# Kernel tuning notes

Hardware: AMD Instinct MI355X
Metric: run time of the kernel (lower is better)

The kernel has to match this reference:

```python
import jax, jax.numpy as jnp
import numpy as np

RHO = 1.0
L = 50
RS = np.array([20, 40, 80, 160], dtype=np.int32)

def _get_index():
    S = []
    for m in range(-L // 2, L // 2 + 1):
        for n in range(-L // 2, L // 2 + 1):
            if abs(m * n) <= RHO * L // 2:
                S.append((m, n))
    return np.array(S, dtype=np.int32)

IDX = _get_index()          # [449, 2] (m, n) pairs
K = IDX.shape[0]            # 449
B, N, M = 8, 65536, 2       # batch, sequence length, Nmodes (dual-pol)


def setup_inputs() -> dict:
    key = jax.random.key(0)
    ks = jax.random.split(key, 8)
    shp = (B, N, M)
    inp = {
        "E_real": jax.random.normal(ks[0], shp, jnp.float32),
        "E_imag": jax.random.normal(ks[1], shp, jnp.float32),
        "F_real": jax.random.normal(ks[2], shp, jnp.float32),
        "F_imag": jax.random.normal(ks[3], shp, jnp.float32),
        "C1_real": jax.random.normal(ks[4], (len(RS), K), jnp.float32) * 0.01,
        "C1_imag": jax.random.normal(ks[5], (len(RS), K), jnp.float32) * 0.01,
        "C2_real": jax.random.normal(ks[6], (len(RS), K), jnp.float32) * 0.01,
        "C2_imag": jax.random.normal(ks[7], (len(RS), K), jnp.float32) * 0.01,
    }
    # task_info columns: (P [dBm], Fi, Fs [Hz], Nch); Fs must be 2e9 * some Rs entry
    ti = np.zeros((B, 4), dtype=np.float32)
    ti[:, 0] = 2.0
    ti[:, 2] = RS[np.arange(B) % len(RS)].astype(np.float32) * 2e9
    inp["task_info"] = jnp.asarray(ti)
    return inp


def _forward(E_real, E_imag, F_real, F_imag, C1_real, C1_imag, C2_real, C2_imag, task_info):
    E = E_real + 1j * E_imag    # [B, N, M] complex64
    F = F_real + 1j * F_imag

    # choose_C: map Fs -> row of C tables (sorted-Rs order, as in the torch code)
    rs_sorted = jnp.sort(jnp.asarray(RS))
    x = (task_info[:, 2] / 2e9).astype(jnp.int32)              # [B]
    ind = jnp.argmax(x[:, None] == rs_sorted[None, :], axis=-1)  # [B]
    C1 = (C1_real + 1j * C1_imag)[ind]                         # [B, K]
    C2 = (C2_real + 1j * C2_imag)[ind]                         # [B, K]

    ms = jnp.asarray(IDX[:, 0])
    ns = jnp.asarray(IDX[:, 1])

    def step(acc, xs):
        m, n, c1, c2 = xs                                       # c1, c2: [B]
        En  = jnp.roll(E, n, axis=-2)
        Em  = jnp.roll(E, m, axis=-2)
        Emn = jnp.roll(E, m + n, axis=-2)
        Fn  = jnp.roll(F, n, axis=-2)
        Fmn = jnp.roll(F, m + n, axis=-2)
        A = En * jnp.conj(Fmn) * c1[:, None, None] + Fn * jnp.conj(Emn) * c2[:, None, None]
        # (A + A.roll(1, dim=-1)) swaps/combines the two polarizations
        return acc + (A + jnp.roll(A, 1, axis=-1)) * Em, None

    acc, _ = jax.lax.scan(step, jnp.zeros_like(E), (ms, ns, C1.T, C2.T))

    P = jnp.power(10.0, task_info[:, 0] / 10.0) / E.shape[-1]   # [B]
    Eo = F + (jnp.sqrt(P) ** 3)[:, None, None] * acc
    return E[:, L:-L, :], Eo[:, L:-L, :]


def reference(E_real, E_imag, F_real, F_imag, C1_real, C1_imag, C2_real, C2_imag, task_info):
    return _forward(E_real, E_imag, F_real, F_imag,
                    C1_real, C1_imag, C2_real, C2_imag, task_info)
```

## Files before the change

### kernel.cpp

```cpp
#include <hip/hip_runtime.h>
#include <hip/hip_bf16.h>


namespace {

constexpr int NSEQ    = 65536;
constexpr int BATCH   = 8;
constexpr int KTAPS   = 449;
constexpr int NM      = 25;
constexpr int THREADS = 256;
constexpr int TILE    = 1024;
constexpr int WIN     = TILE + 4 * NM;
constexpr int WINQ    = WIN / 4;
constexpr int GHW     = TILE + 2 * NM + 1;
constexpr int GHH     = (GHW + 1) / 2;

typedef float v2f __attribute__((ext_vector_type(2)));

__device__ inline v2f pkfma(float s, v2f v, v2f acc) {
  return __builtin_elementwise_fma((v2f){s, s}, v, acc);
}

__device__ inline void mac(v2f& U13, v2f& U42, v2f& V13, v2f& V42,
                           const float4 c, const float4 g) {
  const v2f glo = (v2f){g.x, g.y}, ghi = (v2f){g.z, g.w};
  U13 = pkfma(c.x, glo, U13); U42 = pkfma(c.y, glo, U42);
  V13 = pkfma(c.z, ghi, V13); V42 = pkfma(c.w, ghi, V42);
}

__device__ inline unsigned short f2bf(float f) {
  __hip_bfloat16 h = __float2bfloat16(f);
  union { __hip_bfloat16 hh; unsigned short u; } cv;
  cv.hh = h;
  return cv.u;
}

__global__ void prep_c_kernel(const float* __restrict__ c1r, const float* __restrict__ c1i,
                              const float* __restrict__ c2r, const float* __restrict__ c2i,
                              float4* __restrict__ cw) {
  int idx = blockIdx.x * blockDim.x + threadIdx.x;
  if (idx < 4 * KTAPS) {
    cw[idx]             = make_float4(c1r[idx], c1i[idx], c2r[idx], c2i[idx]);
    cw[4 * KTAPS + idx] = make_float4(c2r[idx], c2i[idx], c1r[idx], c1i[idx]);
  }
}

__device__ inline float4 gh_entry(const float4 e, const float4 f,
                                  const float4 fm, const float4 em) {
  v2f G = (v2f){fm.w * e.w, fm.w * (-e.z)};
  G = pkfma(fm.x, (v2f){e.x, e.y}, G);
  G = pkfma(fm.y, (v2f){e.y, -e.x}, G);
  G = pkfma(fm.z, (v2f){e.z, e.w}, G);
  v2f H = (v2f){em.w * f.w, em.w * (-f.z)};
  H = pkfma(em.x, (v2f){f.x, f.y}, H);
  H = pkfma(em.y, (v2f){f.y, -f.x}, H);
  H = pkfma(em.z, (v2f){f.z, f.w}, H);
  return make_float4(G.x, G.y, H.x, H.y);
}

template<int NMAX>
__device__ inline void fir4(const float4* __restrict__ A0, const float4* __restrict__ A1,
                            int b0, int b1, const float4* __restrict__ cc,
                            v2f* __restrict__ acc )
{
  constexpr int T = 2 * NMAX + 1;
  float4 cw0, cw1, cw2, cw3;
#pragma unroll
  for (int s = 0; s <= T + 2; ++s) {
    const float4 g = (s & 1) ? A1[b1 - (s >> 1)] : A0[b0 - (s >> 1)];
    if (s < T) cw0 = cc[s];
    if (s <= T - 1)           mac(acc[12], acc[13], acc[14], acc[15], cw0, g);
    if (s >= 1 && s <= T)     mac(acc[ 8], acc[ 9], acc[10], acc[11], cw1, g);
    if (s >= 2 && s <= T + 1) mac(acc[ 4], acc[ 5], acc[ 6], acc[ 7], cw2, g);
    if (s >= 3)               mac(acc[ 0], acc[ 1], acc[ 2], acc[ 3], cw3, g);
    cw3 = cw2; cw2 = cw1; cw1 = cw0;
  }
}

#define FIR_SWITCH(NMX, A0_, A1_, B0_, B1_, CC, ACC) \
  switch (NMX) { \
    case 25: fir4<25>(A0_, A1_, B0_, B1_, CC, ACC); break; \
    case 12: fir4<12>(A0_, A1_, B0_, B1_, CC, ACC); break; \
    case  8: fir4< 8>(A0_, A1_, B0_, B1_, CC, ACC); break; \
    case  6: fir4< 6>(A0_, A1_, B0_, B1_, CC, ACC); break; \
    case  5: fir4< 5>(A0_, A1_, B0_, B1_, CC, ACC); break; \
    case  4: fir4< 4>(A0_, A1_, B0_, B1_, CC, ACC); break; \
    case  3: fir4< 3>(A0_, A1_, B0_, B1_, CC, ACC); break; \
    case  2: fir4< 2>(A0_, A1_, B0_, B1_, CC, ACC); break; \
    default: fir4< 1>(A0_, A1_, B0_, B1_, CC, ACC); break; \
  }

__global__ __launch_bounds__(THREADS, 2) void hpbc_kernel(
    const float2* __restrict__ er, const float2* __restrict__ ei,
    const float2* __restrict__ fr, const float2* __restrict__ fi,
    const float*  __restrict__ task, const float4* __restrict__ cw,
    unsigned short* __restrict__ out, int nout, int lpad, int ntiles)
{
  __shared__ float4 sE4[4][WINQ];
  __shared__ float4 sF[WIN];
  __shared__ float4 ghE0[GHH], ghO0[GHH];
  __shared__ float4 ghE1[GHH], ghO1[GHH];

  const int bx   = blockIdx.x;
  const int b    = bx / ntiles;
  const int tile = bx - b * ntiles;
  const int tid  = threadIdx.x;
  const int i0   = lpad + tile * TILE;
  const int elo  = i0 - 2 * NM;

  const float2* erb = er + (size_t)b * NSEQ;
  const float2* eib = ei + (size_t)b * NSEQ;
  const float2* frb = fr + (size_t)b * NSEQ;
  const float2* fib = fi + (size_t)b * NSEQ;

  for (int u = tid; u < WIN; u += THREADS) {
    int g = (elo + u) & (NSEQ - 1);
    float2 a = erb[g], c = eib[g];
    sE4[u & 3][u >> 2] = make_float4(a.x, c.x, a.y, c.y);
    float2 d = frb[g], e = fib[g];
    sF[u] = make_float4(d.x, e.x, d.y, e.y);
  }

  const float dbm = task[b * 4 + 0];
  const float fsr = task[b * 4 + 2];
  const int   x   = (int)(fsr / 2.0e9f);
  const int ind = (x == 40) ? 1 : (x == 80) ? 2 : (x == 160) ? 3 : 0;
  const float4* __restrict__ crow = cw + ind * KTAPS;
  const float4* __restrict__ cswp = cw + 4 * KTAPS + ind * KTAPS;
  const float P  = powf(10.0f, dbm * 0.1f) * 0.5f;
  const float pf = P * sqrtf(P);

  __syncthreads();

  const int pE = (tid + NM) & 3, iE = (tid + NM) >> 2;
  float4 eH[5], fH[5];
#pragma unroll
  for (int k = 0; k < 4; ++k) { eH[k] = sE4[pE][iE + 64 * k]; fH[k] = sF[tid + NM + 256 * k]; }
  const bool has5 = tid < GHW - 4 * THREADS;
  if (has5) { eH[4] = sE4[pE][iE + 256]; fH[4] = sF[tid + NM + 1024]; }

  auto write_gh = [&](float4* wE, float4* wO, int Mn) {
    const int s  = NM - Mn;
    const int pS = (tid + s) & 3, iS = (tid + s) >> 2;
    const int wi = tid >> 1;
#pragma unroll
    for (int k = 0; k < 4; ++k) {
      const float4 fm = sF[tid + s + 256 * k];
      const float4 em = sE4[pS][iS + 64 * k];
      const float4 gk = gh_entry(eH[k], fH[k], fm, em);
      if (tid & 1) wO[wi + 128 * k] = gk; else wE[wi + 128 * k] = gk;
    }
    if (has5) {
      const float4 fm = sF[tid + s + 1024];
      const float4 em = sE4[pS][iS + 256];
      const float4 gk = gh_entry(eH[4], fH[4], fm, em);
      if (tid & 1) wO[wi + 512] = gk; else wE[wi + 512] = gk;
    }
  };

  v2f O0[4], O1[4];
#pragma unroll
  for (int r = 0; r < 4; ++r) { O0[r] = (v2f){0, 0}; O1[r] = (v2f){0, 0}; }
  int kbaseP = 199, kbaseN = 199;

  auto iter = [&](const float4* rE, const float4* rO,
                  float4* wE, float4* wO, int M) {
    const int nmax = (M == 0) ? NM : (NM / M);
    const int T    = 2 * nmax + 1;

    {
      const int X = 28 + nmax;
      const float4* A0 = (X & 1) ? rO : rE;
      const float4* A1 = (X & 1) ? rE : rO;
      const int b0 = 2 * tid + (X >> 1);
      const int b1 = 2 * tid + ((X - 1) >> 1);
      v2f acc[16];
#pragma unroll
      for (int j = 0; j < 16; ++j) acc[j] = (v2f){0, 0};
      FIR_SWITCH(nmax, A0, A1, b0, b1, crow + kbaseP, acc);
      kbaseP += T;
#pragma unroll
      for (int r = 0; r < 4; ++r) {
        const float sr = acc[4*r].x - acc[4*r+1].y + acc[4*r+2].x - acc[4*r+3].y;
        const float si = acc[4*r].y + acc[4*r+1].x + acc[4*r+2].y + acc[4*r+3].x;
        const int u = 4 * tid + r + 2 * NM - M;
        const float4 e = sE4[u & 3][u >> 2];
        O0[r] = pkfma(sr, (v2f){e.x, e.y}, pkfma(si, (v2f){-e.y, e.x}, O0[r]));
        O1[r] = pkfma(sr, (v2f){e.z, e.w}, pkfma(si, (v2f){-e.w, e.z}, O1[r]));
      }
    }

    if (M > 0) {
      kbaseN -= T;
      const int X = 28 + nmax + M;
      const float4* A0 = (X & 1) ? rO : rE;
      const float4* A1 = (X & 1) ? rE : rO;
      const int b0 = 2 * tid + (X >> 1);
      const int b1 = 2 * tid + ((X - 1) >> 1);
      v2f acc[16];
#pragma unroll
      for (int j = 0; j < 16; ++j) acc[j] = (v2f){0, 0};
      FIR_SWITCH(nmax, A0, A1, b0, b1, cswp + kbaseN, acc);
#pragma unroll
      for (int r = 0; r < 4; ++r) {
        const float sr = acc[4*r].x + acc[4*r+1].y + acc[4*r+2].x + acc[4*r+3].y;
        const float si = acc[4*r+1].x - acc[4*r].y + acc[4*r+3].x - acc[4*r+2].y;
        const int u = 4 * tid + r + 2 * NM + M;
        const float4 e = sE4[u & 3][u >> 2];
        O0[r] = pkfma(sr, (v2f){e.x, e.y}, pkfma(si, (v2f){-e.y, e.x}, O0[r]));
        O1[r] = pkfma(sr, (v2f){e.z, e.w}, pkfma(si, (v2f){-e.w, e.z}, O1[r]));
      }
    }

    if (M < NM) write_gh(wE, wO, M + 1);
    __syncthreads();
  };

  write_gh(ghE0, ghO0, 0);
  __syncthreads();

  for (int M = 0; M <= NM; M += 2) {
    iter(ghE0, ghO0, ghE1, ghO1, M);
    if (M + 1 <= NM)
      iter(ghE1, ghO1, ghE0, ghO0, M + 1);
  }

  const int end = lpad + nout;
  const size_t chunk1 = (size_t)BATCH * nout * 4;
#pragma unroll
  for (int r = 0; r < 4; ++r) {
    const int ii = 4 * tid + r;
    const int i  = i0 + ii;
    if (i < end) {
      const int u = ii + 2 * NM;
      const float4 ev = sE4[u & 3][u >> 2];
      const float4 fv = sF[u];
      const size_t o = ((size_t)b * nout + (size_t)(i - lpad)) * 4;
      ushort4 w0, w1;
      w0.x = f2bf(ev.y); w0.y = f2bf(ev.x); w0.z = f2bf(ev.w); w0.w = f2bf(ev.z);
      w1.x = f2bf(fv.y + pf * O0[r].y); w1.y = f2bf(fv.x + pf * O0[r].x);
      w1.z = f2bf(fv.w + pf * O1[r].y); w1.w = f2bf(fv.z + pf * O1[r].x);
      *reinterpret_cast<ushort4*>(out + o) = w0;
      *reinterpret_cast<ushort4*>(out + chunk1 + o) = w1;
    }
  }
}

}

extern "C" void kernel_launch(void* const* d_in, const int* in_sizes, int n_in,
                              void* d_out, int out_size, void* d_ws, size_t ws_size,
                              hipStream_t stream) {
  const float* E_real  = (const float*)d_in[0];
  const float* E_imag  = (const float*)d_in[1];
  const float* F_real  = (const float*)d_in[2];
  const float* F_imag  = (const float*)d_in[3];
  const float* C1_real = (const float*)d_in[4];
  const float* C1_imag = (const float*)d_in[5];
  const float* C2_real = (const float*)d_in[6];
  const float* C2_imag = (const float*)d_in[7];
  const float* task    = (const float*)d_in[8];

  int nout = out_size / 32;
  if (nout < 1 || nout > NSEQ) nout = NSEQ - 100;
  const int lpad   = (NSEQ - nout) / 2;
  const int ntiles = (nout + TILE - 1) / TILE;

  unsigned short* outp = (unsigned short*)d_out;
  float4* cw = (float4*)d_ws;

  hipLaunchKernelGGL(prep_c_kernel, dim3((4 * KTAPS + 255) / 256), dim3(256), 0, stream,
                     C1_real, C1_imag, C2_real, C2_imag, cw);

  hipLaunchKernelGGL(hpbc_kernel, dim3(BATCH * ntiles), dim3(THREADS), 0, stream,
                     (const float2*)E_real, (const float2*)E_imag,
                     (const float2*)F_real, (const float2*)F_imag,
                     task, cw, outp, nout, lpad, ntiles);
}
```

Measured before the change: 82.97 us.

## Store GH buffers in four-way phase-split layout and slide E window in registers

The intermediate G/H arrays in shared memory go from a two-way even/odd split to a four-way phase split indexed by position mod 4. Each thread's FIR reads then become unit-stride across lanes, which is meant to cut LDS bank conflicts and remove the per-tap pointer select. The E values used to multiply the FIR outputs are now kept in a register sliding window, so each iteration loads two new entries instead of four. This costs a few more registers and more index arithmetic for the four base offsets.

```diff
diff --git a/kernel.cpp b/kernel.cpp
--- a/kernel.cpp
+++ b/kernel.cpp
@@ -13,7 +13,7 @@
 constexpr int WIN     = TILE + 4 * NM;
 constexpr int WINQ    = WIN / 4;
 constexpr int GHW     = TILE + 2 * NM + 1;
-constexpr int GHH     = (GHW + 1) / 2;
+constexpr int GHQ     = (GHW + 3) / 4;
 
 typedef float v2f __attribute__((ext_vector_type(2)));
 
@@ -59,15 +59,18 @@
 }
 
 template<int NMAX>
-__device__ inline void fir4(const float4* __restrict__ A0, const float4* __restrict__ A1,
-                            int b0, int b1, const float4* __restrict__ cc,
+__device__ inline void fir4(const float4* __restrict__ gh,
+                            int B0, int B1, int B2, int B3,
+                            const float4* __restrict__ cc,
                             v2f* __restrict__ acc )
 {
   constexpr int T = 2 * NMAX + 1;
   float4 cw0, cw1, cw2, cw3;
 #pragma unroll
   for (int s = 0; s <= T + 2; ++s) {
-    const float4 g = (s & 1) ? A1[b1 - (s >> 1)] : A0[b0 - (s >> 1)];
+    const int q = s & 3, a = s >> 2;
+    const int base = (q == 0) ? B0 : (q == 1) ? B1 : (q == 2) ? B2 : B3;
+    const float4 g = gh[base - a];
     if (s < T) cw0 = cc[s];
     if (s <= T - 1)           mac(acc[12], acc[13], acc[14], acc[15], cw0, g);
     if (s >= 1 && s <= T)     mac(acc[ 8], acc[ 9], acc[10], acc[11], cw1, g);
@@ -77,17 +80,17 @@
   }
 }
 
-#define FIR_SWITCH(NMX, A0_, A1_, B0_, B1_, CC, ACC) \
+#define FIR_SWITCH(NMX, GH_, B0_, B1_, B2_, B3_, CC, ACC) \
   switch (NMX) { \
-    case 25: fir4<25>(A0_, A1_, B0_, B1_, CC, ACC); break; \
-    case 12: fir4<12>(A0_, A1_, B0_, B1_, CC, ACC); break; \
-    case  8: fir4< 8>(A0_, A1_, B0_, B1_, CC, ACC); break; \
-    case  6: fir4< 6>(A0_, A1_, B0_, B1_, CC, ACC); break; \
-    case  5: fir4< 5>(A0_, A1_, B0_, B1_, CC, ACC); break; \
-    case  4: fir4< 4>(A0_, A1_, B0_, B1_, CC, ACC); break; \
-    case  3: fir4< 3>(A0_, A1_, B0_, B1_, CC, ACC); break; \
-    case  2: fir4< 2>(A0_, A1_, B0_, B1_, CC, ACC); break; \
-    default: fir4< 1>(A0_, A1_, B0_, B1_, CC, ACC); break; \
+    case 25: fir4<25>(GH_, B0_, B1_, B2_, B3_, CC, ACC); break; \
+    case 12: fir4<12>(GH_, B0_, B1_, B2_, B3_, CC, ACC); break; \
+    case  8: fir4< 8>(GH_, B0_, B1_, B2_, B3_, CC, ACC); break; \
+    case  6: fir4< 6>(GH_, B0_, B1_, B2_, B3_, CC, ACC); break; \
+    case  5: fir4< 5>(GH_, B0_, B1_, B2_, B3_, CC, ACC); break; \
+    case  4: fir4< 4>(GH_, B0_, B1_, B2_, B3_, CC, ACC); break; \
+    case  3: fir4< 3>(GH_, B0_, B1_, B2_, B3_, CC, ACC); break; \
+    case  2: fir4< 2>(GH_, B0_, B1_, B2_, B3_, CC, ACC); break; \
+    default: fir4< 1>(GH_, B0_, B1_, B2_, B3_, CC, ACC); break; \
   }
 
 __global__ __launch_bounds__(THREADS, 2) void hpbc_kernel(
@@ -98,8 +101,8 @@
 {
   __shared__ float4 sE4[4][WINQ];
   __shared__ float4 sF[WIN];
-  __shared__ float4 ghE0[GHH], ghO0[GHH];
-  __shared__ float4 ghE1[GHH], ghO1[GHH];
+  __shared__ float4 ghA[4 * GHQ];
+  __shared__ float4 ghB[4 * GHQ];
 
   const int bx   = blockIdx.x;
   const int b    = bx / ntiles;
@@ -139,22 +142,21 @@
   const bool has5 = tid < GHW - 4 * THREADS;
   if (has5) { eH[4] = sE4[pE][iE + 256]; fH[4] = sF[tid + NM + 1024]; }
 
-  auto write_gh = [&](float4* wE, float4* wO, int Mn) {
+  const int wbase = (tid & 3) * GHQ + (tid >> 2);
+
+  auto write_gh = [&](float4* wGH, int Mn) {
     const int s  = NM - Mn;
     const int pS = (tid + s) & 3, iS = (tid + s) >> 2;
-    const int wi = tid >> 1;
 #pragma unroll
     for (int k = 0; k < 4; ++k) {
       const float4 fm = sF[tid + s + 256 * k];
       const float4 em = sE4[pS][iS + 64 * k];
-      const float4 gk = gh_entry(eH[k], fH[k], fm, em);
-      if (tid & 1) wO[wi + 128 * k] = gk; else wE[wi + 128 * k] = gk;
+      wGH[wbase + 64 * k] = gh_entry(eH[k], fH[k], fm, em);
     }
     if (has5) {
       const float4 fm = sF[tid + s + 1024];
       const float4 em = sE4[pS][iS + 256];
-      const float4 gk = gh_entry(eH[4], fH[4], fm, em);
-      if (tid & 1) wO[wi + 512] = gk; else wE[wi + 512] = gk;
+      wGH[wbase + 256] = gh_entry(eH[4], fH[4], fm, em);
     }
   };
 
@@ -163,28 +165,34 @@
   for (int r = 0; r < 4; ++r) { O0[r] = (v2f){0, 0}; O1[r] = (v2f){0, 0}; }
   int kbaseP = 199, kbaseN = 199;
 
-  auto iter = [&](const float4* rE, const float4* rO,
-                  float4* wE, float4* wO, int M) {
+  float4 W_p[4], W_m[4];
+#pragma unroll
+  for (int r = 0; r < 4; ++r) {
+    const int u = 4 * tid + r + 2 * NM;
+    W_p[r] = sE4[u & 3][u >> 2];
+    W_m[r] = W_p[r];
+  }
+
+  auto iter = [&](const float4* rGH, float4* wGH, int M) {
     const int nmax = (M == 0) ? NM : (NM / M);
     const int T    = 2 * nmax + 1;
 
     {
       const int X = 28 + nmax;
-      const float4* A0 = (X & 1) ? rO : rE;
-      const float4* A1 = (X & 1) ? rE : rO;
-      const int b0 = 2 * tid + (X >> 1);
-      const int b1 = 2 * tid + ((X - 1) >> 1);
+      const int B0 = ((X    ) & 3) * GHQ + tid + ((X    ) >> 2);
+      const int B1 = ((X - 1) & 3) * GHQ + tid + ((X - 1) >> 2);
+      const int B2 = ((X - 2) & 3) * GHQ + tid + ((X - 2) >> 2);
+      const int B3 = ((X - 3) & 3) * GHQ + tid + ((X - 3) >> 2);
       v2f acc[16];
 #pragma unroll
       for (int j = 0; j < 16; ++j) acc[j] = (v2f){0, 0};
-      FIR_SWITCH(nmax, A0, A1, b0, b1, crow + kbaseP, acc);
+      FIR_SWITCH(nmax, rGH, B0, B1, B2, B3, crow + kbaseP, acc);
       kbaseP += T;
 #pragma unroll
       for (int r = 0; r < 4; ++r) {
         const float sr = acc[4*r].x - acc[4*r+1].y + acc[4*r+2].x - acc[4*r+3].y;
         const float si = acc[4*r].y + acc[4*r+1].x + acc[4*r+2].y + acc[4*r+3].x;
-        const int u = 4 * tid + r + 2 * NM - M;
-        const float4 e = sE4[u & 3][u >> 2];
+        const float4 e = W_p[r];
         O0[r] = pkfma(sr, (v2f){e.x, e.y}, pkfma(si, (v2f){-e.y, e.x}, O0[r]));
         O1[r] = pkfma(sr, (v2f){e.z, e.w}, pkfma(si, (v2f){-e.w, e.z}, O1[r]));
       }
@@ -193,36 +201,45 @@
     if (M > 0) {
       kbaseN -= T;
       const int X = 28 + nmax + M;
-      const float4* A0 = (X & 1) ? rO : rE;
-      const float4* A1 = (X & 1) ? rE : rO;
-      const int b0 = 2 * tid + (X >> 1);
-      const int b1 = 2 * tid + ((X - 1) >> 1);
+      const int B0 = ((X    ) & 3) * GHQ + tid + ((X    ) >> 2);
+      const int B1 = ((X - 1) & 3) * GHQ + tid + ((X - 1) >> 2);
+      const int B2 = ((X - 2) & 3) * GHQ + tid + ((X - 2) >> 2);
+      const int B3 = ((X - 3) & 3) * GHQ + tid + ((X - 3) >> 2);
       v2f acc[16];
 #pragma unroll
       for (int j = 0; j < 16; ++j) acc[j] = (v2f){0, 0};
-      FIR_SWITCH(nmax, A0, A1, b0, b1, cswp + kbaseN, acc);
+      FIR_SWITCH(nmax, rGH, B0, B1, B2, B3, cswp + kbaseN, acc);
 #pragma unroll
       for (int r = 0; r < 4; ++r) {
         const float sr = acc[4*r].x + acc[4*r+1].y + acc[4*r+2].x + acc[4*r+3].y;
         const float si = acc[4*r+1].x - acc[4*r].y + acc[4*r+3].x - acc[4*r+2].y;
-        const int u = 4 * tid + r + 2 * NM + M;
-        const float4 e = sE4[u & 3][u >> 2];
+        const float4 e = W_m[r];
         O0[r] = pkfma(sr, (v2f){e.x, e.y}, pkfma(si, (v2f){-e.y, e.x}, O0[r]));
         O1[r] = pkfma(sr, (v2f){e.z, e.w}, pkfma(si, (v2f){-e.w, e.z}, O1[r]));
       }
     }
 
-    if (M < NM) write_gh(wE, wO, M + 1);
+    if (M < NM) write_gh(wGH, M + 1);
+
+    {
+      const int up = 4 * tid + 2 * NM - (M + 1);
+      W_p[3] = W_p[2]; W_p[2] = W_p[1]; W_p[1] = W_p[0];
+      W_p[0] = sE4[up & 3][up >> 2];
+      const int um = 4 * tid + 3 + 2 * NM + (M + 1);
+      W_m[0] = W_m[1]; W_m[1] = W_m[2]; W_m[2] = W_m[3];
+      W_m[3] = sE4[um & 3][um >> 2];
+    }
+
     __syncthreads();
   };
 
-  write_gh(ghE0, ghO0, 0);
+  write_gh(ghA, 0);
   __syncthreads();
 
   for (int M = 0; M <= NM; M += 2) {
-    iter(ghE0, ghO0, ghE1, ghO1, M);
+    iter(ghA, ghB, M);
     if (M + 1 <= NM)
-      iter(ghE1, ghO1, ghE0, ghO0, M + 1);
+      iter(ghB, ghA, M + 1);
   }
 
   const int end = lpad + nout;
```

After: 83.98 us. No clear change (+1.2%).
